# Optimization experiments

Hardware: AMD Instinct MI355X
Metric: run time of the kernel (lower is better)

Reference implementation:

```python
import jax, jax.numpy as jnp
import numpy as np

N = 50000          # nodes
E = 800000         # edges (avg degree 16)
FEAT = 128         # self.feat_dim
MAX_SPK = 3
SPK_DIM = 16
SPA_DIM = 16
OUT = 64


def _lin(key, din, dout):
    kw, kb = jax.random.split(key)
    w = jax.random.normal(kw, (din, dout), dtype=jnp.float32) * (1.0 / np.sqrt(din))
    b = jax.random.normal(kb, (dout,), dtype=jnp.float32) * 0.01
    return w, b


def setup_inputs() -> dict:
    key = jax.random.key(0)
    ks = jax.random.split(key, 16)
    D = 7 * FEAT + 5  # 901
    x = jax.random.normal(ks[0], (N, D), dtype=jnp.float32)
    # last column is a speaker count in {1..4} (clamped to max 3 in forward)
    num_spk = jax.random.randint(ks[1], (N,), 1, 5).astype(jnp.float32)
    x = x.at[:, -1].set(num_spk)
    edge_index = jax.random.randint(ks[2], (2, E), 0, N, dtype=jnp.int32)
    edge_attr = jnp.zeros((E,), dtype=jnp.int32)  # all pass the (==111)|(==0) filter

    speaker_w, speaker_b = _lin(ks[3], MAX_SPK, SPK_DIM)
    spatial_w, spatial_b = _lin(ks[4], 4, SPA_DIM)
    # face_trans params
    f1_w, f1_b = _lin(ks[5], FEAT, OUT)
    f2_w, f2_b = _lin(ks[6], FEAT + SPK_DIM + SPA_DIM, OUT)
    fe_w, fe_b = _lin(ks[7], 2 * OUT, 2)
    # face_body_trans params
    g1_w, g1_b = _lin(ks[8], FEAT, OUT)
    g2_w, g2_b = _lin(ks[9], FEAT + SPK_DIM + SPA_DIM, OUT)
    ge_w, ge_b = _lin(ks[10], 2 * OUT, 2)
    return dict(x=x, edge_index=edge_index, edge_attr=edge_attr,
                speaker_w=speaker_w, speaker_b=speaker_b,
                spatial_w=spatial_w, spatial_b=spatial_b,
                f1_w=f1_w, f1_b=f1_b, f2_w=f2_w, f2_b=f2_b, fe_w=fe_w, fe_b=fe_b,
                g1_w=g1_w, g1_b=g1_b, g2_w=g2_w, g2_b=g2_b, ge_w=ge_w, ge_b=ge_b)


def _edge_conv(h, src, dst, valid, ew, eb):
    # PyG EdgeConv (aggr='max'): out_i = max_j MLP([x_i, x_j - x_i])
    hi = h[dst]                                   # [E, 64]
    hj = h[src]                                   # [E, 64]
    msg = jnp.concatenate([hi, hj - hi], axis=1) @ ew + eb  # [E, 2]
    msg = jnp.where(valid[:, None], msg, -jnp.inf)
    out = jax.ops.segment_max(msg, dst, num_segments=h.shape[0])
    return jnp.where(jnp.isfinite(out), out, 0.0)  # empty segments -> 0 (PyG fill)


def reference(x, edge_index, edge_attr,
              speaker_w, speaker_b, spatial_w, spatial_b,
              f1_w, f1_b, f2_w, f2_b, fe_w, fe_b,
              g1_w, g1_b, g2_w, g2_b, ge_w, ge_b):
    valid = (edge_attr == 111) | (edge_attr == 0)
    src, dst = edge_index[0], edge_index[1]

    # speaker-count embedding: one_hot(clamp(x[:,-1]-1, max=2)) -> Linear(3,16)
    spk_idx = jnp.minimum(x[:, -1] - 1.0, MAX_SPK - 1).astype(jnp.int32)
    spk = jax.nn.one_hot(spk_idx, MAX_SPK, dtype=x.dtype) @ speaker_w + speaker_b
    spa = x[:, -5:-1] @ spatial_w + spatial_b

    def block(feat, fc1_w, fc1_b, fc2_w, fc2_b, ew, eb):
        # dropout p=0.9 is identity in eval mode
        h = (feat @ fc1_w + fc1_b) + (jnp.concatenate([feat, spk, spa], axis=1) @ fc2_w + fc2_b)
        return _edge_conv(h, src, dst, valid, ew, eb)

    o_face = block(x[:, :FEAT], f1_w, f1_b, f2_w, f2_b, fe_w, fe_b)
    o_body = block(x[:, FEAT:2 * FEAT], g1_w, g1_b, g2_w, g2_b, ge_w, ge_b)
    return o_face + o_body
```

## Files before the change

### kernel.cpp

```cpp
#include <hip/hip_runtime.h>
#include <hip/hip_bf16.h>
#include <math.h>

#define ROWLEN 901
#define NEGENC 0x007FFFFFu
#define CNTSTRIDE 8

__device__ __forceinline__ unsigned encf(float f) {
    unsigned u = __float_as_uint(f);
    return (u & 0x80000000u) ? ~u : (u | 0x80000000u);
}
__device__ __forceinline__ float decf(unsigned u) {
    return (u & 0x80000000u) ? __uint_as_float(u ^ 0x80000000u)
                             : __uint_as_float(~u);
}

__global__ __launch_bounds__(256) void k_compose(
    const float* __restrict__ spkw, const float* __restrict__ spkb,
    const float* __restrict__ spaw, const float* __restrict__ spab,
    const float* __restrict__ f1w, const float* __restrict__ f1b,
    const float* __restrict__ f2w, const float* __restrict__ f2b,
    const float* __restrict__ few, const float* __restrict__ feb,
    const float* __restrict__ g1w, const float* __restrict__ g1b,
    const float* __restrict__ g2w, const float* __restrict__ g2b,
    const float* __restrict__ gew, const float* __restrict__ geb,
    float* __restrict__ C, float* __restrict__ Sp,
    float* __restrict__ Tab, float* __restrict__ Cst)
{
    const int t = threadIdx.x;

    if (blockIdx.x < 16) {
        const int row = blockIdx.x * 16 + (t >> 4);
        const int kk  = t & 15;
        const int blk = row >> 7;
        const int fr  = row & 127;
        const float* w1 = blk ? g1w : f1w;
        const float* w2 = blk ? g2w : f2w;
        const float* e  = blk ? gew : few;

        const float4 wa = *(const float4*)(w1 + fr * 64 + kk * 4);
        const float4 wb = *(const float4*)(w2 + fr * 64 + kk * 4);
        const float wv[4] = {wa.x + wb.x, wa.y + wb.y, wa.z + wb.z, wa.w + wb.w};

        float a0 = 0.f, a1 = 0.f, a2 = 0.f, a3 = 0.f;
        #pragma unroll
        for (int j = 0; j < 4; ++j) {
            const int k = kk * 4 + j;
            const float eb0 = e[(64 + k) * 2 + 0];
            const float eb1 = e[(64 + k) * 2 + 1];
            const float ea0 = e[k * 2 + 0] - eb0;
            const float ea1 = e[k * 2 + 1] - eb1;
            a0 += wv[j] * ea0; a1 += wv[j] * ea1;
            a2 += wv[j] * eb0; a3 += wv[j] * eb1;
        }
        #pragma unroll
        for (int m = 1; m <= 8; m <<= 1) {
            a0 += __shfl_xor(a0, m, 64);
            a1 += __shfl_xor(a1, m, 64);
            a2 += __shfl_xor(a2, m, 64);
            a3 += __shfl_xor(a3, m, 64);
        }
        if (kk == 0) {
            C[row * 4 + 0] = a0; C[row * 4 + 1] = a1;
            C[row * 4 + 2] = a2; C[row * 4 + 3] = a3;
        }
        return;
    }

    __shared__ float sEW[2][256];
    __shared__ float sUV[2][2][2][16][2];
    __shared__ float sBE[8][8];

    sEW[0][t] = few[t];
    sEW[1][t] = gew[t];
    __syncthreads();

    {
        const int c    = t & 1;
        const int k16  = (t >> 1) & 15;
        const int role = (t >> 5) & 1;
        const int blk  = (t >> 6) & 1;
        const int isV  = (t >> 7) & 1;
        const float* w2 = blk ? g2w : f2w;
        const float* e  = sEW[blk];
        const int row = (isV ? 144 : 128) + k16;
        float acc = 0.f;
        #pragma unroll
        for (int k4 = 0; k4 < 16; ++k4) {
            const float4 w = *(const float4*)(w2 + row * 64 + k4 * 4);
            const float wv[4] = {w.x, w.y, w.z, w.w};
            #pragma unroll
            for (int j = 0; j < 4; ++j) {
                const int k = k4 * 4 + j;
                const float ev = role ? e[(64 + k) * 2 + c]
                                      : (e[k * 2 + c] - e[(64 + k) * 2 + c]);
                acc += wv[j] * ev;
            }
        }
        sUV[isV][blk][role][k16][c] = acc;
    }

    if (t < 64) {
        const int combo = t >> 3;
        const int part  = t & 7;
        const int c = combo & 1, role = (combo >> 1) & 1, blk = combo >> 2;
        const float* b1 = blk ? g1b : f1b;
        const float* b2 = blk ? g2b : f2b;
        const float* e  = sEW[blk];
        float acc = 0.f;
        #pragma unroll
        for (int j = 0; j < 8; ++j) {
            const int k = part * 8 + j;
            const float ev = role ? e[(64 + k) * 2 + c]
                                  : (e[k * 2 + c] - e[(64 + k) * 2 + c]);
            acc += (b1[k] + b2[k]) * ev;
        }
        sBE[combo][part] = acc;
    }
    __syncthreads();

    if (t < 24) {
        const int blk = t / 12, rem = t % 12;
        const int idx = rem >> 2, q = rem & 3;
        const int role = q >> 1, c = q & 1;
        float acc = 0.f;
        #pragma unroll
        for (int k = 0; k < 16; ++k)
            acc += spkw[idx * 16 + k] * sUV[0][blk][role][k][c];
        Tab[blk * 12 + idx * 4 + q] = acc;
    } else if (t >= 32 && t < 64) {
        const int u = t - 32;
        const int blk = u >> 4, rem = u & 15;
        const int r = rem >> 2, q = rem & 3;
        const int role = q >> 1, c = q & 1;
        float acc = 0.f;
        #pragma unroll
        for (int k = 0; k < 16; ++k)
            acc += spaw[r * 16 + k] * sUV[1][blk][role][k][c];
        Sp[blk * 16 + r * 4 + q] = acc;
    } else if (t >= 64 && t < 72) {
        const int u = t - 64;
        const int blk = u >> 2, q = u & 3;
        const int role = q >> 1, c = q & 1;
        const float* ebv = blk ? geb : feb;
        float acc = (role == 0) ? ebv[c] : 0.f;
        #pragma unroll
        for (int k = 0; k < 16; ++k) {
            acc += spkb[k] * sUV[0][blk][role][k][c];
            acc += spab[k] * sUV[1][blk][role][k][c];
        }
        #pragma unroll
        for (int p = 0; p < 8; ++p) acc += sBE[u][p];
        Cst[blk * 4 + q] = acc;
    }
}

__global__ __launch_bounds__(256) void k_node(
    const float* __restrict__ x,
    const float* __restrict__ C, const float* __restrict__ Sp,
    const float* __restrict__ Tab, const float* __restrict__ Cst,
    float4* __restrict__ Adat, float4* __restrict__ Bdat,
    unsigned* __restrict__ maxbuf, int* __restrict__ cnt, int nnodes)
{
    const int wave = threadIdx.x >> 6;
    const int lane = threadIdx.x & 63;
    const int node = blockIdx.x * 4 + wave;
    if (node >= nnodes) return;

    const float* xr = x + (size_t)node * ROWLEN;
    const int half = lane >> 5;
    const int l32  = lane & 31;
    const float* xh = xr + half * 128;
    const float4* C4 = (const float4*)C;

    float xs0 = 0.f, xs1 = 0.f, xs2 = 0.f, xs3 = 0.f, xspk = 0.f;
    if (lane == 0) {
        xs0 = xr[896]; xs1 = xr[897]; xs2 = xr[898]; xs3 = xr[899];
        xspk = xr[900];
    }

    float a0 = 0.f, a1 = 0.f, a2 = 0.f, a3 = 0.f;
    #pragma unroll
    for (int k = 0; k < 4; ++k) {
        const int el = l32 + 32 * k;
        const float v = xh[el];
        const float4 cr = C4[half * 128 + el];
        a0 += v * cr.x; a1 += v * cr.y; a2 += v * cr.z; a3 += v * cr.w;
    }

    #pragma unroll
    for (int m = 16; m >= 1; m >>= 1) {
        a0 += __shfl_xor(a0, m, 64);
        a1 += __shfl_xor(a1, m, 64);
        a2 += __shfl_xor(a2, m, 64);
        a3 += __shfl_xor(a3, m, 64);
    }
    const float b0 = __shfl(a0, 32, 64);
    const float b1 = __shfl(a1, 32, 64);
    const float b2 = __shfl(a2, 32, 64);
    const float b3 = __shfl(a3, 32, 64);

    if (lane == 0) {
        const float xs[4] = {xs0, xs1, xs2, xs3};
        int idx = (int)fminf(xspk - 1.0f, 2.0f);
        idx = idx < 0 ? 0 : (idx > 2 ? 2 : idx);

        const float pq[2][4] = {{a0, a1, a2, a3}, {b0, b1, b2, b3}};
        float av[4], bv[4];
        #pragma unroll
        for (int blk = 0; blk < 2; ++blk) {
            #pragma unroll
            for (int c = 0; c < 2; ++c) {
                float ea = Tab[blk * 12 + idx * 4 + c] + Cst[blk * 4 + c];
                float eb = Tab[blk * 12 + idx * 4 + 2 + c] + Cst[blk * 4 + 2 + c];
                #pragma unroll
                for (int r = 0; r < 4; ++r) {
                    ea += xs[r] * Sp[blk * 16 + r * 4 + c];
                    eb += xs[r] * Sp[blk * 16 + r * 4 + 2 + c];
                }
                av[blk * 2 + c] = pq[blk][c] + ea;
                bv[blk * 2 + c] = pq[blk][2 + c] + eb;
            }
        }
        Adat[node] = make_float4(av[0], av[1], av[2], av[3]);
        Bdat[node] = make_float4(bv[0], bv[1], bv[2], bv[3]);
        *(uint4*)(maxbuf + (size_t)node * 4) =
            make_uint4(NEGENC, NEGENC, NEGENC, NEGENC);
        cnt[(size_t)node * CNTSTRIDE] = 0;
    }
}

__global__ __launch_bounds__(256) void k_scatter(
    const int* __restrict__ ei, const int* __restrict__ ea,
    const float4* __restrict__ Bdat,
    int* __restrict__ cnt, int* __restrict__ bucket,
    unsigned* __restrict__ maxbuf, int nedges, int cap)
{
    const int e = blockIdx.x * blockDim.x + threadIdx.x;
    if (e >= nedges) return;
    const int attr = ea[e];
    if (!(attr == 0 || attr == 111)) return;
    const int s = ei[e];
    const int d = ei[nedges + e];
    const int pos = atomicAdd(cnt + (size_t)d * CNTSTRIDE, 1);
    if (pos < cap) {
        bucket[(size_t)d * cap + pos] = s;
    } else {
        const float4 b = Bdat[s];
        unsigned* mb = maxbuf + (size_t)d * 4;
        atomicMax(mb + 0, encf(b.x));
        atomicMax(mb + 1, encf(b.y));
        atomicMax(mb + 2, encf(b.z));
        atomicMax(mb + 3, encf(b.w));
    }
}

__global__ __launch_bounds__(256) void k_gather(
    const float4* __restrict__ Adat, const float4* __restrict__ Bdat,
    const int* __restrict__ cnt, const int* __restrict__ bucket,
    const unsigned* __restrict__ maxbuf,
    float* __restrict__ out, int nnodes, int cap)
{
    const int t = blockIdx.x * blockDim.x + threadIdx.x;
    const int n = t >> 2, sub = t & 3;
    if (n >= nnodes) return;
    int c = cnt[(size_t)n * CNTSTRIDE]; if (c > cap) c = cap;

    float m0 = -INFINITY, m1 = -INFINITY, m2 = -INFINITY, m3 = -INFINITY;
    const int* row = bucket + (size_t)n * cap;
    int i = sub;
    int s_next = (i < c) ? row[i] : 0;
    while (i < c) {
        const int s = s_next;
        i += 4;
        if (i < c) s_next = row[i];
        const float4 b = Bdat[s];
        m0 = fmaxf(m0, b.x); m1 = fmaxf(m1, b.y);
        m2 = fmaxf(m2, b.z); m3 = fmaxf(m3, b.w);
    }
    #pragma unroll
    for (int msk = 1; msk <= 2; msk <<= 1) {
        m0 = fmaxf(m0, __shfl_xor(m0, msk, 64));
        m1 = fmaxf(m1, __shfl_xor(m1, msk, 64));
        m2 = fmaxf(m2, __shfl_xor(m2, msk, 64));
        m3 = fmaxf(m3, __shfl_xor(m3, msk, 64));
    }
    if (sub == 0) {
        const uint4 ov = *(const uint4*)(maxbuf + (size_t)n * 4);
        m0 = fmaxf(m0, decf(ov.x)); m1 = fmaxf(m1, decf(ov.y));
        m2 = fmaxf(m2, decf(ov.z)); m3 = fmaxf(m3, decf(ov.w));
        const float4 a = Adat[n];
        const float f0 = isfinite(m0) ? a.x + m0 : 0.f;
        const float f1 = isfinite(m1) ? a.y + m1 : 0.f;
        const float f2 = isfinite(m2) ? a.z + m2 : 0.f;
        const float f3 = isfinite(m3) ? a.w + m3 : 0.f;
        out[(size_t)n * 2 + 0] = f0 + f2;
        out[(size_t)n * 2 + 1] = f1 + f3;
    }
}

extern "C" void kernel_launch(void* const* d_in, const int* in_sizes, int n_in,
                              void* d_out, int out_size, void* d_ws, size_t ws_size,
                              hipStream_t stream) {
    const float* x    = (const float*)d_in[0];
    const int*   ei   = (const int*)d_in[1];
    const int*   ea   = (const int*)d_in[2];
    const float* spkw = (const float*)d_in[3];
    const float* spkb = (const float*)d_in[4];
    const float* spaw = (const float*)d_in[5];
    const float* spab = (const float*)d_in[6];
    const float* f1w  = (const float*)d_in[7];
    const float* f1b  = (const float*)d_in[8];
    const float* f2w  = (const float*)d_in[9];
    const float* f2b  = (const float*)d_in[10];
    const float* few  = (const float*)d_in[11];
    const float* feb  = (const float*)d_in[12];
    const float* g1w  = (const float*)d_in[13];
    const float* g1b  = (const float*)d_in[14];
    const float* g2w  = (const float*)d_in[15];
    const float* g2b  = (const float*)d_in[16];
    const float* gew  = (const float*)d_in[17];
    const float* geb  = (const float*)d_in[18];

    const int N = in_sizes[0] / ROWLEN;
    const int E = in_sizes[2];

    char* ws = (char*)d_ws;
    float*    C      = (float*)(ws + 0);
    float*    Sp     = (float*)(ws + 4096);
    float*    Tab    = (float*)(ws + 4096 + 128);
    float*    Cst    = (float*)(ws + 4096 + 256);
    size_t off = 16384;
    float4*   Adat   = (float4*)(ws + off);   off += (size_t)N * 16;
    float4*   Bdat   = (float4*)(ws + off);   off += (size_t)N * 16;
    unsigned* maxbuf = (unsigned*)(ws + off); off += (size_t)N * 16;
    int*      cnt    = (int*)(ws + off);      off += (((size_t)N * CNTSTRIDE * 4 + 255) / 256) * 256;
    int*      bucket = (int*)(ws + off);
    const size_t remain = ws_size > off ? ws_size - off : 0;
    size_t cap_sz = remain / ((size_t)N * 4);
    int CAP = cap_sz > 64 ? 64 : (int)cap_sz;

    k_compose<<<17, 256, 0, stream>>>(spkw, spkb, spaw, spab,
                                      f1w, f1b, f2w, f2b, few, feb,
                                      g1w, g1b, g2w, g2b, gew, geb,
                                      C, Sp, Tab, Cst);

    k_node<<<(N + 3) / 4, 256, 0, stream>>>(x, C, Sp, Tab, Cst,
                                            Adat, Bdat, maxbuf, cnt, N);

    k_scatter<<<(E + 255) / 256, 256, 0, stream>>>(ei, ea, Bdat, cnt, bucket,
                                                   maxbuf, E, CAP);

    k_gather<<<((size_t)N * 4 + 255) / 256, 256, 0, stream>>>(Adat, Bdat, cnt, bucket,
                                                              maxbuf, (float*)d_out, N, CAP);
}
```

Baseline: 321.5 us.

## Fuse edge scatter with node transform kernel and replace atomic-max overflow with spill list

The edge bucketing scatter no longer waits for Bdat: it now runs in the same launch as the per-node projection, using dedicated blocks, so edge-index traffic overlaps the large x-row reads. Zeroing the counters moves into extra blocks of the compose kernel. Overflow edges go to a global spill list instead of atomicMax on encoded floats, which removes the maxbuf buffer. The gather kernel scans the whole spill list for every node when it is non-empty, which could be costly if overflow ever happens.

```diff
diff --git a/kernel.cpp b/kernel.cpp
--- a/kernel.cpp
+++ b/kernel.cpp
@@ -3,17 +3,9 @@
 #include <math.h>
 
 #define ROWLEN 901
-#define NEGENC 0x007FFFFFu
 #define CNTSTRIDE 8
-
-__device__ __forceinline__ unsigned encf(float f) {
-    unsigned u = __float_as_uint(f);
-    return (u & 0x80000000u) ? ~u : (u | 0x80000000u);
-}
-__device__ __forceinline__ float decf(unsigned u) {
-    return (u & 0x80000000u) ? __uint_as_float(u ^ 0x80000000u)
-                             : __uint_as_float(~u);
-}
+#define NB_SC 512
+#define ZB 96
 
 __global__ __launch_bounds__(256) void k_compose(
     const float* __restrict__ spkw, const float* __restrict__ spkb,
@@ -25,9 +17,19 @@
     const float* __restrict__ g2w, const float* __restrict__ g2b,
     const float* __restrict__ gew, const float* __restrict__ geb,
     float* __restrict__ C, float* __restrict__ Sp,
-    float* __restrict__ Tab, float* __restrict__ Cst)
+    float* __restrict__ Tab, float* __restrict__ Cst,
+    uint4* __restrict__ cntz, int nCntQuads, int* __restrict__ spillcnt)
 {
     const int t = threadIdx.x;
+
+    if (blockIdx.x >= 17) {
+        const int zid = blockIdx.x - 17;
+        if (zid == 0 && t == 0) *spillcnt = 0;
+        const uint4 z = make_uint4(0u, 0u, 0u, 0u);
+        for (int i = zid * 256 + t; i < nCntQuads; i += ZB * 256)
+            cntz[i] = z;
+        return;
+    }
 
     if (blockIdx.x < 16) {
         const int row = blockIdx.x * 16 + (t >> 4);
@@ -155,16 +157,37 @@
     }
 }
 
-__global__ __launch_bounds__(256) void k_node(
+__global__ __launch_bounds__(256) void k_fused(
     const float* __restrict__ x,
     const float* __restrict__ C, const float* __restrict__ Sp,
     const float* __restrict__ Tab, const float* __restrict__ Cst,
-    float4* __restrict__ Adat, float4* __restrict__ Bdat,
-    unsigned* __restrict__ maxbuf, int* __restrict__ cnt, int nnodes)
+    float4* __restrict__ Adat, float4* __restrict__ Bdat, int nnodes,
+    const int* __restrict__ ei, const int* __restrict__ ea,
+    int* __restrict__ cnt, int* __restrict__ bucket,
+    int* __restrict__ spillcnt, int* __restrict__ spill,
+    int nedges, int cap)
 {
+    if (blockIdx.x < NB_SC) {
+        for (int e = blockIdx.x * 256 + threadIdx.x; e < nedges; e += NB_SC * 256) {
+            const int attr = ea[e];
+            if (!(attr == 0 || attr == 111)) continue;
+            const int s = ei[e];
+            const int d = ei[nedges + e];
+            const int pos = atomicAdd(cnt + (size_t)d * CNTSTRIDE, 1);
+            if (pos < cap) {
+                bucket[(size_t)d * cap + pos] = s;
+            } else {
+                const int sp = atomicAdd(spillcnt, 1);
+                spill[2 * sp + 0] = d;
+                spill[2 * sp + 1] = s;
+            }
+        }
+        return;
+    }
+
     const int wave = threadIdx.x >> 6;
     const int lane = threadIdx.x & 63;
-    const int node = blockIdx.x * 4 + wave;
+    const int node = (blockIdx.x - NB_SC) * 4 + wave;
     if (node >= nnodes) return;
 
     const float* xr = x + (size_t)node * ROWLEN;
@@ -211,54 +234,26 @@
         for (int blk = 0; blk < 2; ++blk) {
             #pragma unroll
             for (int c = 0; c < 2; ++c) {
-                float ea = Tab[blk * 12 + idx * 4 + c] + Cst[blk * 4 + c];
-                float eb = Tab[blk * 12 + idx * 4 + 2 + c] + Cst[blk * 4 + 2 + c];
+                float ea_ = Tab[blk * 12 + idx * 4 + c] + Cst[blk * 4 + c];
+                float eb_ = Tab[blk * 12 + idx * 4 + 2 + c] + Cst[blk * 4 + 2 + c];
                 #pragma unroll
                 for (int r = 0; r < 4; ++r) {
-                    ea += xs[r] * Sp[blk * 16 + r * 4 + c];
-                    eb += xs[r] * Sp[blk * 16 + r * 4 + 2 + c];
+                    ea_ += xs[r] * Sp[blk * 16 + r * 4 + c];
+                    eb_ += xs[r] * Sp[blk * 16 + r * 4 + 2 + c];
                 }
-                av[blk * 2 + c] = pq[blk][c] + ea;
-                bv[blk * 2 + c] = pq[blk][2 + c] + eb;
+                av[blk * 2 + c] = pq[blk][c] + ea_;
+                bv[blk * 2 + c] = pq[blk][2 + c] + eb_;
             }
         }
         Adat[node] = make_float4(av[0], av[1], av[2], av[3]);
         Bdat[node] = make_float4(bv[0], bv[1], bv[2], bv[3]);
-        *(uint4*)(maxbuf + (size_t)node * 4) =
-            make_uint4(NEGENC, NEGENC, NEGENC, NEGENC);
-        cnt[(size_t)node * CNTSTRIDE] = 0;
-    }
-}
-
-__global__ __launch_bounds__(256) void k_scatter(
-    const int* __restrict__ ei, const int* __restrict__ ea,
-    const float4* __restrict__ Bdat,
-    int* __restrict__ cnt, int* __restrict__ bucket,
-    unsigned* __restrict__ maxbuf, int nedges, int cap)
-{
-    const int e = blockIdx.x * blockDim.x + threadIdx.x;
-    if (e >= nedges) return;
-    const int attr = ea[e];
-    if (!(attr == 0 || attr == 111)) return;
-    const int s = ei[e];
-    const int d = ei[nedges + e];
-    const int pos = atomicAdd(cnt + (size_t)d * CNTSTRIDE, 1);
-    if (pos < cap) {
-        bucket[(size_t)d * cap + pos] = s;
-    } else {
-        const float4 b = Bdat[s];
-        unsigned* mb = maxbuf + (size_t)d * 4;
-        atomicMax(mb + 0, encf(b.x));
-        atomicMax(mb + 1, encf(b.y));
-        atomicMax(mb + 2, encf(b.z));
-        atomicMax(mb + 3, encf(b.w));
     }
 }
 
 __global__ __launch_bounds__(256) void k_gather(
     const float4* __restrict__ Adat, const float4* __restrict__ Bdat,
     const int* __restrict__ cnt, const int* __restrict__ bucket,
-    const unsigned* __restrict__ maxbuf,
+    const int* __restrict__ spillcnt, const int* __restrict__ spill,
     float* __restrict__ out, int nnodes, int cap)
 {
     const int t = blockIdx.x * blockDim.x + threadIdx.x;
@@ -278,6 +273,18 @@
         m0 = fmaxf(m0, b.x); m1 = fmaxf(m1, b.y);
         m2 = fmaxf(m2, b.z); m3 = fmaxf(m3, b.w);
     }
+
+    const int ns = *spillcnt;
+    if (ns > 0) {
+        for (int j = sub; j < ns; j += 4) {
+            if (spill[2 * j] == n) {
+                const float4 b = Bdat[spill[2 * j + 1]];
+                m0 = fmaxf(m0, b.x); m1 = fmaxf(m1, b.y);
+                m2 = fmaxf(m2, b.z); m3 = fmaxf(m3, b.w);
+            }
+        }
+    }
+
     #pragma unroll
     for (int msk = 1; msk <= 2; msk <<= 1) {
         m0 = fmaxf(m0, __shfl_xor(m0, msk, 64));
@@ -286,9 +293,6 @@
         m3 = fmaxf(m3, __shfl_xor(m3, msk, 64));
     }
     if (sub == 0) {
-        const uint4 ov = *(const uint4*)(maxbuf + (size_t)n * 4);
-        m0 = fmaxf(m0, decf(ov.x)); m1 = fmaxf(m1, decf(ov.y));
-        m2 = fmaxf(m2, decf(ov.z)); m3 = fmaxf(m3, decf(ov.w));
         const float4 a = Adat[n];
         const float f0 = isfinite(m0) ? a.x + m0 : 0.f;
         const float f1 = isfinite(m1) ? a.y + m1 : 0.f;
@@ -333,24 +337,30 @@
     size_t off = 16384;
     float4*   Adat   = (float4*)(ws + off);   off += (size_t)N * 16;
     float4*   Bdat   = (float4*)(ws + off);   off += (size_t)N * 16;
-    unsigned* maxbuf = (unsigned*)(ws + off); off += (size_t)N * 16;
-    int*      cnt    = (int*)(ws + off);      off += (((size_t)N * CNTSTRIDE * 4 + 255) / 256) * 256;
+    size_t cntBytes  = (((size_t)N * CNTSTRIDE * 4 + 255) / 256) * 256;
+    int*      cnt    = (int*)(ws + off);      off += cntBytes;
+    int*      spillcnt = (int*)(ws + off);    off += 256;
+    int*      spill  = (int*)(ws + off);      off += (((size_t)E * 8 + 255) / 256) * 256;
     int*      bucket = (int*)(ws + off);
     const size_t remain = ws_size > off ? ws_size - off : 0;
     size_t cap_sz = remain / ((size_t)N * 4);
     int CAP = cap_sz > 64 ? 64 : (int)cap_sz;
 
-    k_compose<<<17, 256, 0, stream>>>(spkw, spkb, spaw, spab,
-                                      f1w, f1b, f2w, f2b, few, feb,
-                                      g1w, g1b, g2w, g2b, gew, geb,
-                                      C, Sp, Tab, Cst);
-
-    k_node<<<(N + 3) / 4, 256, 0, stream>>>(x, C, Sp, Tab, Cst,
-                                            Adat, Bdat, maxbuf, cnt, N);
-
-    k_scatter<<<(E + 255) / 256, 256, 0, stream>>>(ei, ea, Bdat, cnt, bucket,
-                                                   maxbuf, E, CAP);
+    const int nCntQuads = (int)(cntBytes / 16);
+
+    k_compose<<<17 + ZB, 256, 0, stream>>>(spkw, spkb, spaw, spab,
+                                           f1w, f1b, f2w, f2b, few, feb,
+                                           g1w, g1b, g2w, g2b, gew, geb,
+                                           C, Sp, Tab, Cst,
+                                           (uint4*)cnt, nCntQuads, spillcnt);
+
+    const int NB_ND = (N + 3) / 4;
+    k_fused<<<NB_SC + NB_ND, 256, 0, stream>>>(x, C, Sp, Tab, Cst,
+                                               Adat, Bdat, N,
+                                               ei, ea, cnt, bucket,
+                                               spillcnt, spill, E, CAP);
 
     k_gather<<<((size_t)N * 4 + 255) / 256, 256, 0, stream>>>(Adat, Bdat, cnt, bucket,
-                                                              maxbuf, (float*)d_out, N, CAP);
+                                                              spillcnt, spill,
+                                                              (float*)d_out, N, CAP);
 }
```

After: 314.8 us. 1.02x faster.
